# Kernel tuning notes

Measured on AMD Instinct MI355X. Metric: run time of the kernel, lower is better.

The kernel has to match this reference:

```python
import jax, jax.numpy as jnp
import numpy as np

EPS = 1e-5

# 8 corner sign patterns (matching torch A..H order) and inclusion-exclusion coeffs
_SIGNS = np.array([[ 1, 1, 1],   # A  +
                   [ 1, 1,-1],   # B  -
                   [ 1,-1, 1],   # C  -
                   [-1, 1, 1],   # D  -
                   [ 1,-1,-1],   # E  +
                   [-1,-1, 1],   # F  +
                   [-1, 1,-1],   # G  +
                   [-1,-1,-1]],  # H  -
                  dtype=np.float32)
_COEFFS = np.prod(_SIGNS, axis=-1).astype(np.float32)


def _trilinear_border(vol, coords):
    """vol: [C,D,H,W]; coords: [d,h,w,3] normalized (x,y,z) in [-1,1],
    align_corners=True, padding_mode='border'. Returns [C,d,h,w]."""
    C, D, H, W = vol.shape
    ix = jnp.clip((coords[..., 0] + 1.0) * 0.5 * (W - 1), 0.0, W - 1)
    iy = jnp.clip((coords[..., 1] + 1.0) * 0.5 * (H - 1), 0.0, H - 1)
    iz = jnp.clip((coords[..., 2] + 1.0) * 0.5 * (D - 1), 0.0, D - 1)
    x0 = jnp.floor(ix); y0 = jnp.floor(iy); z0 = jnp.floor(iz)
    fx = ix - x0; fy = iy - y0; fz = iz - z0
    x0i = jnp.clip(x0.astype(jnp.int32), 0, W - 1); x1i = jnp.clip(x0i + 1, 0, W - 1)
    y0i = jnp.clip(y0.astype(jnp.int32), 0, H - 1); y1i = jnp.clip(y0i + 1, 0, H - 1)
    z0i = jnp.clip(z0.astype(jnp.int32), 0, D - 1); z1i = jnp.clip(z0i + 1, 0, D - 1)
    out = jnp.zeros((C,) + ix.shape, dtype=vol.dtype)
    for zi, wz in ((z0i, 1.0 - fz), (z1i, fz)):
        for yi, wy in ((y0i, 1.0 - fy), (y1i, fy)):
            for xi, wx in ((x0i, 1.0 - fx), (x1i, fx)):
                out = out + vol[:, zi, yi, xi] * (wz * wy * wx)[None]
    return out


def setup_inputs() -> dict:
    key = jax.random.key(0)
    k1, k2 = jax.random.split(key)
    x = jax.random.normal(k1, (2, 4, 64, 128, 128), dtype=jnp.float32)
    kernel_sizes = jax.random.uniform(k2, (2, 64, 128, 128, 3), dtype=jnp.float32,
                                      minval=1.0, maxval=9.0)
    return {"x": x, "kernel_sizes": kernel_sizes}


def reference(x, kernel_sizes):
    N, C, D, H, W = x.shape
    d, h, w = D, H, W  # out_size = None -> input spatial size
    mean = jnp.mean(x, axis=(-3, -2, -1), keepdims=True)
    std = jnp.std(x, axis=(-3, -2, -1), keepdims=True, ddof=1)  # torch unbiased std
    I = (x - mean) / (std + EPS)
    I = jnp.cumsum(jnp.cumsum(jnp.cumsum(I, axis=-1), axis=-2), axis=-3)  # summed-area table

    gx = jnp.linspace(-1.0, 1.0, w, dtype=x.dtype) - 1.0 / w
    gy = jnp.linspace(-1.0, 1.0, h, dtype=x.dtype) - 1.0 / h
    gz = jnp.linspace(-1.0, 1.0, d, dtype=x.dtype) - 1.0 / d
    grid = jnp.stack(jnp.broadcast_arrays(gx[None, None, :], gy[None, :, None],
                                          gz[:, None, None]), axis=-1)  # [d,h,w,3]

    inv = jnp.array([1.0 / w, 1.0 / h, 1.0 / d], dtype=x.dtype)
    K = kernel_sizes * inv  # [N,D,H,W,3], normalized half-sizes
    signs = jnp.asarray(_SIGNS, dtype=x.dtype)
    coeffs = jnp.asarray(_COEFFS, dtype=x.dtype)
    # grids: [8,N,d,h,w,3]
    grids = grid[None, None] + signs[:, None, None, None, None, :] * K[None]

    sample_corners = jax.vmap(_trilinear_border, in_axes=(None, 0))       # over 8 corners
    sample_batch = jax.vmap(sample_corners, in_axes=(0, 1), out_axes=1)   # over N
    samples = sample_batch(I, grids)  # [8,N,C,d,h,w]

    result = jnp.einsum('s,sncdhw->ncdhw', coeffs, samples)
    area = jnp.prod(kernel_sizes, axis=-1)[:, None]  # [N,1,D,H,W]
    return (result / (area + EPS)) * std + mean
```

## Files before the change

kernel.cpp:

```cpp
#include <hip/hip_runtime.h>
#include <math.h>

constexpr int N = 2, C = 4, D = 64, H = 128, W = 128;
constexpr int HW  = H * W;
constexpr int DHW = D * H * W;
constexpr int NC  = N * C;
constexpr float EPSf = 1e-5f;

constexpr int RX = 17;
constexpr int RXY = RX * RX;
constexpr int RSLOTS = RXY * RX;
constexpr int RCHUNKS = 77;
constexpr int RPAD = RCHUNKS * 64;

typedef const __attribute__((address_space(1))) void glb_void;
typedef __attribute__((address_space(3))) void lds_void;
typedef __attribute__((ext_vector_type(2))) float f32x2;

__global__ __launch_bounds__(256) void k_sat2d(const float* __restrict__ x,
                                               float* __restrict__ sat,
                                               float* __restrict__ pSw,
                                               float* __restrict__ pQw) {
    __shared__ float tile[H * W];
    const int slice = blockIdx.x;
    const int nc = slice >> 6;
    const int z  = slice & 63;
    const int n  = nc >> 2;
    const int c  = nc & 3;
    const float* src = x + (size_t)slice * HW;

    float s = 0.f, q = 0.f;
    for (int i = threadIdx.x; i < HW; i += 256) {
        int y = i >> 7, xx = i & 127;
        float v = src[i];
        s += v; q += v * v;
        tile[(y << 7) + (xx ^ (y & 31))] = v;
    }
    #pragma unroll
    for (int off = 32; off; off >>= 1) {
        s += __shfl_down(s, off, 64);
        q += __shfl_down(q, off, 64);
    }
    if ((threadIdx.x & 63) == 0) {
        const int w = threadIdx.x >> 6;
        pSw[slice * 4 + w] = s;
        pQw[slice * 4 + w] = q;
    }
    __syncthreads();
    if (threadIdx.x < H) {
        const int y = threadIdx.x;
        const int base = y << 7, sw = y & 31;
        float run = 0.f;
        for (int i = 0; i < W; ++i) {
            int a = base + (i ^ sw);
            run += tile[a];
            tile[a] = run;
        }
    }
    __syncthreads();
    if (threadIdx.x < W) {
        const int xx = threadIdx.x;
        float* dst = sat + ((size_t)(n * D + z) * HW) * 4 + c;
        float run = 0.f;
        for (int y = 0; y < H; ++y) {
            run += tile[(y << 7) + (xx ^ (y & 31))];
            dst[(size_t)(y * W + xx) * 4] = run;
        }
    }
}

__global__ __launch_bounds__(64) void k_stats(const float* __restrict__ pSw,
                                              const float* __restrict__ pQw,
                                              float* __restrict__ stats) {
    const int nc = blockIdx.x;
    const int t  = threadIdx.x;
    const float4 sv = *(const float4*)(pSw + (size_t)(nc * 64 + t) * 4);
    const float4 qv = *(const float4*)(pQw + (size_t)(nc * 64 + t) * 4);
    double s = (double)sv.x + sv.y + sv.z + sv.w;
    double q = (double)qv.x + qv.y + qv.z + qv.w;
    #pragma unroll
    for (int off = 32; off; off >>= 1) {
        s += __shfl_down(s, off, 64);
        q += __shfl_down(q, off, 64);
    }
    if (t == 0) {
        const double M = (double)DHW;
        double mean = s / M;
        double var  = (q - s * s / M) / (M - 1.0);
        float stdv  = (float)sqrt(var);
        stats[nc]     = (float)mean;
        stats[8 + nc] = stdv / (stdv + EPSf);
    }
}

__device__ __forceinline__ void taps4(float g, float K, float scale, int lastI,
                                      int* idx, float* wt) {
    float c  = g - K;
    float ix = fminf(fmaxf((c + 1.0f) * scale, 0.0f), (float)lastI);
    float fl = floorf(ix);
    int   i0 = (int)fl;
    float f  = ix - fl;
    idx[0] = i0; idx[1] = min(i0 + 1, lastI);
    wt[0] = -(1.0f - f); wt[1] = -f;
    c  = g + K;
    ix = fminf(fmaxf((c + 1.0f) * scale, 0.0f), (float)lastI);
    fl = floorf(ix);
    i0 = (int)fl;
    f  = ix - fl;
    idx[2] = i0; idx[3] = min(i0 + 1, lastI);
    wt[2] = 1.0f - f; wt[3] = f;
}

__global__ __launch_bounds__(512) void k_sample(const float4* __restrict__ sat,
                                                const float* __restrict__ ks,
                                                const float* __restrict__ stats,
                                                float* __restrict__ out) {
    extern __shared__ float4 tile[];
    const int bid = (blockIdx.x & 7) * 512 + (blockIdx.x >> 3);
    const int tx = bid & 15, ty = (bid >> 4) & 15, tz = (bid >> 8) & 7;
    const int n  = bid >> 11;
    const int x0 = tx * 8, y0 = ty * 8, z0 = tz * 8;
    const int rx0 = x0 - 5, ry0 = y0 - 5, rz0 = z0 - 5;

    const int lane = threadIdx.x & 63;
    const int wid  = threadIdx.x >> 6;
    const float4* satn = sat + (size_t)n * DHW;

    for (int chunk = wid; chunk < RCHUNKS; chunk += 8) {
        int idx  = chunk * 64 + lane;
        int cidx = min(idx, RSLOTS - 1);
        int rz  = cidx / RXY;
        int rem = cidx - rz * RXY;
        int ry  = rem / RX;
        int rx  = rem - ry * RX;
        int gz = min(max(rz0 + rz, 0), D - 1);
        int gy = min(max(ry0 + ry, 0), H - 1);
        int gx = min(max(rx0 + rx, 0), W - 1);
        const float4* src = satn + ((size_t)gz * HW + (size_t)gy * W + gx);
        __builtin_amdgcn_global_load_lds((glb_void*)src,
                                         (lds_void*)&tile[chunk * 64], 16, 0, 0);
    }
    __syncthreads();

    for (int col = threadIdx.x; col < RXY; col += 512) {
        float4 run = tile[col];
        #pragma unroll
        for (int j = 1; j < RX; ++j) {
            float4 a = tile[j * RXY + col];
            run.x += a.x; run.y += a.y; run.z += a.z; run.w += a.w;
            tile[j * RXY + col] = run;
        }
    }
    __syncthreads();

    const int v = (int)threadIdx.x;
    const int x = x0 + (v & 7);
    const int y = y0 + ((v >> 3) & 7);
    const int z = z0 + (v >> 6);

    const float* kp = ks + (size_t)(((n * D + z) * H + y) * W + x) * 3;
    const float k0 = kp[0], k1 = kp[1], k2 = kp[2];

    const float gx = -1.0f + (float)x * (2.0f / 127.0f) - (1.0f / 128.0f);
    const float gy = -1.0f + (float)y * (2.0f / 127.0f) - (1.0f / 128.0f);
    const float gz = -1.0f + (float)z * (2.0f / 63.0f)  - (1.0f / 64.0f);

    int xi[4], yi[4], zi[4];
    float wx[4], wy[4], wz[4];
    taps4(gx, k0 * (1.0f / 128.0f), 63.5f, 127, xi, wx);
    taps4(gy, k1 * (1.0f / 128.0f), 63.5f, 127, yi, wy);
    taps4(gz, k2 * (1.0f / 64.0f),  31.5f,  63, zi, wz);

    const float cx = wx[0] * (float)(xi[0] + 1) + wx[1] * (float)(xi[1] + 1)
                   + wx[2] * (float)(xi[2] + 1) + wx[3] * (float)(xi[3] + 1);
    const float cy = wy[0] * (float)(yi[0] + 1) + wy[1] * (float)(yi[1] + 1)
                   + wy[2] * (float)(yi[2] + 1) + wy[3] * (float)(yi[3] + 1);
    const float cz = wz[0] * (float)(zi[0] + 1) + wz[1] * (float)(zi[1] + 1)
                   + wz[2] * (float)(zi[2] + 1) + wz[3] * (float)(zi[3] + 1);
    const float cnt = cx * cy * cz;

    const int jx0 = xi[0] - rx0, jx1 = xi[1] - rx0;
    const int jx2 = xi[2] - rx0, jx3 = xi[3] - rx0;
    const f32x2 w0 = {wx[0], wx[0]}, w1 = {wx[1], wx[1]};
    const f32x2 w2 = {wx[2], wx[2]}, w3 = {wx[3], wx[3]};

    f32x2 aL = {0, 0}, aH = {0, 0};
    #pragma unroll
    for (int vv = 0; vv < 4; ++vv) {
        const int   zb  = (zi[vv] - rz0) * RXY;
        const float wzv = wz[vv];
        #pragma unroll
        for (int u = 0; u < 4; ++u) {
            const int rb = zb + (yi[u] - ry0) * RX;
            float4 t0 = tile[rb + jx0];
            float4 t1 = tile[rb + jx1];
            float4 t2 = tile[rb + jx2];
            float4 t3 = tile[rb + jx3];
            f32x2 sL = w0 * f32x2{t0.x, t0.y} + w1 * f32x2{t1.x, t1.y}
                     + w2 * f32x2{t2.x, t2.y} + w3 * f32x2{t3.x, t3.y};
            f32x2 sH = w0 * f32x2{t0.z, t0.w} + w1 * f32x2{t1.z, t1.w}
                     + w2 * f32x2{t2.z, t2.w} + w3 * f32x2{t3.z, t3.w};
            const float wvu = wzv * wy[u];
            const f32x2 ww = {wvu, wvu};
            aL += ww * sL;
            aH += ww * sH;
        }
    }

    const float inva = 1.0f / (k0 * k1 * k2 + EPSf);
    const float4 m4 = *(const float4*)(stats + n * 4);
    const float4 e4 = *(const float4*)(stats + 8 + n * 4);
    const int sb = n * C;
    float* po = out + (size_t)sb * DHW + (size_t)z * HW + y * W + x;
    po[0]               = (aL.x - m4.x * cnt) * (e4.x * inva) + m4.x;
    po[DHW]             = (aL.y - m4.y * cnt) * (e4.y * inva) + m4.y;
    po[2 * (size_t)DHW] = (aH.x - m4.z * cnt) * (e4.z * inva) + m4.z;
    po[3 * (size_t)DHW] = (aH.y - m4.w * cnt) * (e4.w * inva) + m4.w;
}

extern "C" void kernel_launch(void* const* d_in, const int* in_sizes, int n_in,
                              void* d_out, int out_size, void* d_ws, size_t ws_size,
                              hipStream_t stream) {
    const float* x  = (const float*)d_in[0];
    const float* ks = (const float*)d_in[1];
    float* out = (float*)d_out;
    float* ws  = (float*)d_ws;

    float* sat   = ws;
    float* pSw   = ws + (size_t)NC * DHW;
    float* pQw   = pSw + 2048;
    float* stats = pQw + 2048;

    (void)hipFuncSetAttribute((const void*)k_sample,
                              hipFuncAttributeMaxDynamicSharedMemorySize,
                              RPAD * 16);

    k_sat2d <<<NC * D, 256, 0, stream>>>(x, sat, pSw, pQw);
    k_stats <<<NC, 64, 0, stream>>>(pSw, pQw, stats);
    k_sample<<<4096, 512, RPAD * 16, stream>>>((const float4*)sat, ks, stats, out);
}
```

Baseline: 106.7 us.

## Fuse halo load with z-prefix scan and overlap tap computation before barrier

Replaces the async global-to-LDS halo load and the separate in-LDS z-direction prefix pass with a per-column loop that loads 17 z values from global memory into registers and writes running sums straight to LDS. This removes one barrier and a full LDS read/write pass. The per-voxel tap and weight computation now runs before the single barrier, so it overlaps with the loads. Only 289 of 512 threads take part in the load, each with a serial dependent chain of 17 loads, which may expose latency. Launch bounds now request 4 blocks per CU and LDS is sized exactly.

After: 102.8 us. 1.04x faster.

```diff
diff --git a/kernel.cpp b/kernel.cpp
--- a/kernel.cpp
+++ b/kernel.cpp
@@ -10,11 +10,7 @@
 constexpr int RX = 17;
 constexpr int RXY = RX * RX;
 constexpr int RSLOTS = RXY * RX;
-constexpr int RCHUNKS = 77;
-constexpr int RPAD = RCHUNKS * 64;
-
-typedef const __attribute__((address_space(1))) void glb_void;
-typedef __attribute__((address_space(3))) void lds_void;
+
 typedef __attribute__((ext_vector_type(2))) float f32x2;
 
 __global__ __launch_bounds__(256) void k_sat2d(const float* __restrict__ x,
@@ -111,10 +107,10 @@
     wt[2] = 1.0f - f; wt[3] = f;
 }
 
-__global__ __launch_bounds__(512) void k_sample(const float4* __restrict__ sat,
-                                                const float* __restrict__ ks,
-                                                const float* __restrict__ stats,
-                                                float* __restrict__ out) {
+__global__ __launch_bounds__(512, 4) void k_sample(const float4* __restrict__ sat,
+                                                   const float* __restrict__ ks,
+                                                   const float* __restrict__ stats,
+                                                   float* __restrict__ out) {
     extern __shared__ float4 tile[];
     const int bid = (blockIdx.x & 7) * 512 + (blockIdx.x >> 3);
     const int tx = bid & 15, ty = (bid >> 4) & 15, tz = (bid >> 8) & 7;
@@ -122,44 +118,29 @@
     const int x0 = tx * 8, y0 = ty * 8, z0 = tz * 8;
     const int rx0 = x0 - 5, ry0 = y0 - 5, rz0 = z0 - 5;
 
-    const int lane = threadIdx.x & 63;
-    const int wid  = threadIdx.x >> 6;
     const float4* satn = sat + (size_t)n * DHW;
-
-    for (int chunk = wid; chunk < RCHUNKS; chunk += 8) {
-        int idx  = chunk * 64 + lane;
-        int cidx = min(idx, RSLOTS - 1);
-        int rz  = cidx / RXY;
-        int rem = cidx - rz * RXY;
-        int ry  = rem / RX;
-        int rx  = rem - ry * RX;
-        int gz = min(max(rz0 + rz, 0), D - 1);
-        int gy = min(max(ry0 + ry, 0), H - 1);
-        int gx = min(max(rx0 + rx, 0), W - 1);
-        const float4* src = satn + ((size_t)gz * HW + (size_t)gy * W + gx);
-        __builtin_amdgcn_global_load_lds((glb_void*)src,
-                                         (lds_void*)&tile[chunk * 64], 16, 0, 0);
-    }
-    __syncthreads();
-
-    for (int col = threadIdx.x; col < RXY; col += 512) {
-        float4 run = tile[col];
-        #pragma unroll
-        for (int j = 1; j < RX; ++j) {
-            float4 a = tile[j * RXY + col];
-            run.x += a.x; run.y += a.y; run.z += a.z; run.w += a.w;
-            tile[j * RXY + col] = run;
-        }
-    }
-    __syncthreads();
 
     const int v = (int)threadIdx.x;
     const int x = x0 + (v & 7);
     const int y = y0 + ((v >> 3) & 7);
     const int z = z0 + (v >> 6);
-
     const float* kp = ks + (size_t)(((n * D + z) * H + y) * W + x) * 3;
     const float k0 = kp[0], k1 = kp[1], k2 = kp[2];
+
+    for (int col = threadIdx.x; col < RXY; col += 512) {
+        const int ry = col / RX, rx = col - ry * RX;
+        const int gy = min(max(ry0 + ry, 0), H - 1);
+        const int gx = min(max(rx0 + rx, 0), W - 1);
+        const float4* srcp = satn + ((size_t)gy * W + gx);
+        float4 run = {0, 0, 0, 0};
+        #pragma unroll
+        for (int j = 0; j < RX; ++j) {
+            const int gz = min(max(rz0 + j, 0), D - 1);
+            float4 a = srcp[(size_t)gz * HW];
+            run.x += a.x; run.y += a.y; run.z += a.z; run.w += a.w;
+            tile[j * RXY + col] = run;
+        }
+    }
 
     const float gx = -1.0f + (float)x * (2.0f / 127.0f) - (1.0f / 128.0f);
     const float gy = -1.0f + (float)y * (2.0f / 127.0f) - (1.0f / 128.0f);
@@ -183,6 +164,8 @@
     const int jx2 = xi[2] - rx0, jx3 = xi[3] - rx0;
     const f32x2 w0 = {wx[0], wx[0]}, w1 = {wx[1], wx[1]};
     const f32x2 w2 = {wx[2], wx[2]}, w3 = {wx[3], wx[3]};
+
+    __syncthreads();
 
     f32x2 aL = {0, 0}, aH = {0, 0};
     #pragma unroll
@@ -233,9 +216,9 @@
 
     (void)hipFuncSetAttribute((const void*)k_sample,
                               hipFuncAttributeMaxDynamicSharedMemorySize,
-                              RPAD * 16);
+                              RSLOTS * 16);
 
     k_sat2d <<<NC * D, 256, 0, stream>>>(x, sat, pSw, pQw);
     k_stats <<<NC, 64, 0, stream>>>(pSw, pQw, stats);
-    k_sample<<<4096, 512, RPAD * 16, stream>>>((const float4*)sat, ks, stats, out);
-}
+    k_sample<<<4096, 512, RSLOTS * 16, stream>>>((const float4*)sat, ks, stats, out);
+}
```
